# Kernel optimization log

Measured on AMD Instinct MI355X. Metric: run time of the kernel, lower is better.

The kernel has to match this reference:

```python
import jax, jax.numpy as jnp
import numpy as np

DIM = 64
LSH_NUM_PROJS = 7
BLOCK_SIZE = 256
SAMPLE_SIZE = 256
MIN_SEQ_LEN = 2048


def _unit_hamming(n):
    # Gray-code-like permutation used by AngularLSH so adjacent hash ids differ by 1 bit
    a = np.arange(2)
    for i in range(1, n):
        a = np.concatenate([a, a[::-1] + 2 ** i])
    return jnp.asarray(a, dtype=jnp.int32)

_PERM = _unit_hamming(LSH_NUM_PROJS)                                  # [2^P]
_ENC = (2 ** jnp.arange(LSH_NUM_PROJS)).reshape(1, 1, 1, LSH_NUM_PROJS)


def _lsh_hash(mat, proj_dir):
    # mat: [b,h,n,d], proj_dir: [1,1,d,P] -> hash ids [b,h,n]
    mask = jnp.matmul(mat, proj_dir) > 0
    bin_ids = (mask * _ENC).sum(-1)
    return _PERM[bin_ids]


def _exact_attention(q, k, v, scale, causal=False, bias=None):
    qk = jnp.einsum('bhnd,bhmd->bhnm', q, k) * scale
    if causal:
        n, m = q.shape[2], k.shape[2]
        qk = qk + jnp.triu(jnp.full((n, m), jnp.finfo(q.dtype).min, q.dtype), 1)[None, None]
    if bias is not None:
        qk = qk + bias
    lse = jax.scipy.special.logsumexp(qk, axis=-1, keepdims=True)      # [b,h,n,1]
    out = jnp.einsum('bhnm,bhmd->bhnd', jnp.exp(qk - lse), v)
    return out, lse


def _add_attn(a1, l1, a2, l2):
    c = (1.0 / (1.0 + jnp.exp(l2 - l1))).astype(a1.dtype)
    attn = c * a1 + (1 - c) * a2
    lse = l1 - jnp.log(c + jnp.finfo(l1.dtype).eps)
    return attn, lse


def _indexing(x, idx, chunk_size=-1):
    # x: [b,h,n,d], idx: [b,h,s] -> [b,h,s,d] (padded up to a multiple of chunk_size)
    g = jnp.take_along_axis(x, idx[..., None], axis=2)
    n = g.shape[2]
    if chunk_size > 0 and n % chunk_size != 0:
        pad = -n % chunk_size
        g = jnp.pad(g, ((0, 0), (0, 0), (0, pad), (0, 0)))
    return g


def _no_causal(q, k, v, scale, proj_dir, level):
    b, h, n_q, d = q.shape
    n_k = k.shape[2]
    if MIN_SEQ_LEN > n_q:
        return _exact_attention(q, k, v, scale, causal=False)
    q_idx = jnp.argsort(_lsh_hash(q, proj_dir), axis=2)
    k_idx = jnp.argsort(_lsh_hash(k, proj_dir), axis=2)
    q_idx_inv = jnp.argsort(q_idx, axis=2)
    kbs = BLOCK_SIZE
    q_s = _indexing(q, q_idx, kbs)
    k_s = _indexing(k, k_idx, kbs)
    v_s = _indexing(v, k_idx, kbs)
    num_blocks = k_s.shape[2] // kbs
    qbs = q_s.shape[2] // num_blocks
    # block-diagonal attention over LSH-sorted buckets
    q_blk = q_s.reshape(-1, 1, qbs, d)
    k_blk = k_s.reshape(-1, 1, kbs, d)
    v_blk = v_s.reshape(-1, 1, kbs, d)
    attn_block, lse_block = _exact_attention(q_blk, k_blk, v_blk, scale, causal=False)
    attn_block = attn_block.reshape(b, h, q_s.shape[2], -1)
    lse_block = lse_block.reshape(b, h, q_s.shape[2], -1)
    if q_s.shape[2] != n_q:
        attn_block = attn_block[:, :, :n_q, :]
        lse_block = lse_block[:, :, :n_q, :]
        q_s = q_s[:, :, :n_q, :]
        k_s = k_s[:, :, :n_k, :]
        v_s = v_s[:, :, :n_k, :]
    S = SAMPLE_SIZE
    if S > 0 and n_q > qbs and n_k > kbs:
        rng = jax.random.fold_in(jax.random.key(42), level)
        sampled = jax.random.randint(rng, (b, h, S), 0, n_k)
        v_sub = _indexing(v_s, sampled)
        k_sub = _indexing(k_s, sampled)
        offset = jnp.arange(n_q)[None, :, None]                         # (1,n,1)
        bm = (offset // qbs) == (sampled // kbs).reshape(-1, 1, S)      # (b*h,n,S)
        bias = bm.reshape(b, h, n_q, S).astype(q_s.dtype) * jnp.finfo(q_s.dtype).min
        attn_res, lse_res = _exact_attention(q_s, k_sub, v_sub, scale, causal=False, bias=bias)
        lse_res = lse_res + jnp.asarray(np.log(n_k / S), lse_res.dtype)
        attn, lse = _add_attn(attn_block, lse_block, attn_res, lse_res)
    else:
        attn, lse = attn_block, lse_block
    attn = _indexing(attn, q_idx_inv)
    lse = _indexing(lse, q_idx_inv)
    return attn, lse


def _hyper(q, k, v, scale, proj_dir, level=0):
    b, h, n_k, d = k.shape
    n_q = q.shape[2]
    if n_k <= MIN_SEQ_LEN:
        return _exact_attention(q, k, v, scale, causal=True)
    # recursive causal split: block-diagonal halves + un-masked lower-left quadrant
    q_bd = q.reshape(b, 2 * h, n_q // 2, d)
    k_bd = k.reshape(b, 2 * h, n_k // 2, d)
    v_bd = v.reshape(b, 2 * h, n_k // 2, d)
    attn_bd, lse_bd = _hyper(q_bd, k_bd, v_bd, scale, proj_dir, level + 1)
    attn_bd = attn_bd.reshape(b, h, -1, d)
    lse_bd = lse_bd.reshape(b, h, -1, 1)
    a_un, l_un = _no_causal(q[:, :, n_k // 2:, :], k[:, :, :n_k // 2, :],
                            v[:, :, :n_k // 2, :], scale, proj_dir, 100 + level)
    a_up, l_up = attn_bd[:, :, :n_q // 2, :], lse_bd[:, :, :n_q // 2, :]
    a_dn, l_dn = _add_attn(attn_bd[:, :, n_q // 2:, :], lse_bd[:, :, n_q // 2:, :], a_un, l_un)
    return jnp.concatenate([a_up, a_dn], axis=2), jnp.concatenate([l_up, l_dn], axis=2)


def setup_inputs() -> dict:
    rng = jax.random.key(0)
    kq, kk, kv, kp = jax.random.split(rng, 4)
    B, H, N, D = 1, 8, 8192, 64
    return {
        'query': jax.random.normal(kq, (B, H, N, D), jnp.float32),
        'key': jax.random.normal(kk, (B, H, N, D), jnp.float32),
        'value': jax.random.normal(kv, (B, H, N, D), jnp.float32),
        'proj_dir': jax.random.normal(kp, (1, 1, D, LSH_NUM_PROJS), jnp.float32),
    }


def reference(query, key, value, proj_dir):
    scale = query.shape[-1] ** -0.5
    attn, lse = _hyper(query, key, value, scale, proj_dir)
    return attn
```

## Files before the change

### kernel.cpp

```cpp
#include <hip/hip_runtime.h>
#include <stdint.h>
#include <math.h>

#define H 8
#define NSEQ 8192
#define D 64
#define SC2 0.18033688011112042f
#define LN2F 0.69314718055994531f
#define THR2 10.0f
#define EPSF 1.1920928955078125e-07f

typedef short v8s __attribute__((ext_vector_type(8)));
typedef float v4f __attribute__((ext_vector_type(4)));
typedef unsigned short ushort_t;

#define MFMA16(a,b,c) __builtin_amdgcn_mfma_f32_16x16x32_bf16((a),(b),(c),0,0,0)
#define SWZ(row, cb)    (((row)*128) + ((cb) ^ ((((row)&7))<<4)))
#define SWZ256(row, cb) (((row)*256) + ((cb) ^ ((((row)&7))<<4)))

__device__ __forceinline__ float exp2x(float x){
  float r; asm("v_exp_f32 %0, %1" : "=v"(r) : "v"(x)); return r;
}
__device__ __forceinline__ unsigned int cvtpk(float a, float b){
  unsigned int r; asm("v_cvt_pk_bf16_f32 %0, %1, %2" : "=v"(r) : "v"(a), "v"(b)); return r;
}
__device__ __forceinline__ ushort_t f2bf(float f){
  union { float f; unsigned int u; } c; c.f = f;
  unsigned int u = c.u + 0x7FFFu + ((c.u >> 16) & 1u);
  return (ushort_t)(u >> 16);
}
#define VONES (v8s){0x3F80,0x3F80,0x3F80,0x3F80,0x3F80,0x3F80,0x3F80,0x3F80}

__global__ __launch_bounds__(256) void prep_hash(
    const float* __restrict__ q, const float* __restrict__ k, const float* __restrict__ v,
    const float* __restrict__ proj,
    ushort_t* __restrict__ qb, ushort_t* __restrict__ kb, ushort_t* __restrict__ vb,
    int* __restrict__ hq, int* __restrict__ hk)
{
  __shared__ float tile[64][65];
  __shared__ float pj[448];
  __shared__ int pbuf[4][64];
  const int bid = blockIdx.x;
  const int t = threadIdx.x;
  if (bid >= 2048){
    const int tix = bid - 2048;
    size_t off = (size_t)tix*4096 + t*16;
    float4 f0 = *(const float4*)(v + off);
    float4 f1 = *(const float4*)(v + off + 4);
    float4 f2 = *(const float4*)(v + off + 8);
    float4 f3 = *(const float4*)(v + off + 12);
    uint4 o0, o1;
    o0.x = cvtpk(f0.x, f0.y);  o0.y = cvtpk(f0.z, f0.w);
    o0.z = cvtpk(f1.x, f1.y);  o0.w = cvtpk(f1.z, f1.w);
    o1.x = cvtpk(f2.x, f2.y);  o1.y = cvtpk(f2.z, f2.w);
    o1.z = cvtpk(f3.x, f3.y);  o1.w = cvtpk(f3.z, f3.w);
    *(uint4*)(vb + off) = o0;
    *(uint4*)(vb + off + 8) = o1;
    return;
  }
  const int isk = bid & 1;
  const int tix = bid >> 1;
  const int rowbase = tix << 6;
  const float* src = isk ? k : q;
  ushort_t* dstb = isk ? kb : qb;
  int* dsth = isk ? hk : hq;
  for (int i = t; i < 448; i += 256) pj[i] = proj[i];
  {
    const int r = t >> 2, cg = (t & 3) << 4;
    const float* s = src + (size_t)(rowbase + r)*64 + cg;
    float4 f0 = *(const float4*)(s);
    float4 f1 = *(const float4*)(s + 4);
    float4 f2 = *(const float4*)(s + 8);
    float4 f3 = *(const float4*)(s + 12);
    tile[r][cg+0]=f0.x;  tile[r][cg+1]=f0.y;  tile[r][cg+2]=f0.z;  tile[r][cg+3]=f0.w;
    tile[r][cg+4]=f1.x;  tile[r][cg+5]=f1.y;  tile[r][cg+6]=f1.z;  tile[r][cg+7]=f1.w;
    tile[r][cg+8]=f2.x;  tile[r][cg+9]=f2.y;  tile[r][cg+10]=f2.z; tile[r][cg+11]=f2.w;
    tile[r][cg+12]=f3.x; tile[r][cg+13]=f3.y; tile[r][cg+14]=f3.z; tile[r][cg+15]=f3.w;
    uint4 o0, o1;
    o0.x = cvtpk(f0.x, f0.y);  o0.y = cvtpk(f0.z, f0.w);
    o0.z = cvtpk(f1.x, f1.y);  o0.w = cvtpk(f1.z, f1.w);
    o1.x = cvtpk(f2.x, f2.y);  o1.y = cvtpk(f2.z, f2.w);
    o1.z = cvtpk(f3.x, f3.y);  o1.w = cvtpk(f3.z, f3.w);
    *(uint4*)(dstb + (size_t)(rowbase + r)*64 + cg) = o0;
    *(uint4*)(dstb + (size_t)(rowbase + r)*64 + cg + 8) = o1;
  }
  __syncthreads();
  {
    const int r = t & 63, pg = t >> 6;
    const int p2 = (pg < 3) ? (pg + 4) : 6;
    float d0 = 0.0f, d1 = 0.0f;
    for (int d = 0; d < 64; ++d){
      float x = tile[r][d];
      d0 = fmaf(x, pj[d*7 + pg], d0);
      d1 = fmaf(x, pj[d*7 + p2], d1);
    }
    int pb = (d0 > 0.0f ? (1 << pg) : 0);
    if (pg < 3 && d1 > 0.0f) pb |= (1 << (pg + 4));
    pbuf[pg][r] = pb;
  }
  __syncthreads();
  if (t < 64){
    int b = pbuf[0][t] | pbuf[1][t] | pbuf[2][t] | pbuf[3][t];
    dsth[rowbase + t] = b ^ (b >> 1);
  }
}

__device__ __forceinline__ void tf2x32(uint32_t k0, uint32_t k1,
                                       uint32_t x0, uint32_t x1,
                                       uint32_t& o0, uint32_t& o1)
{
  uint32_t ks0 = k0, ks1 = k1, ks2 = k0 ^ k1 ^ 0x1BD11BDAu;
  x0 += ks0; x1 += ks1;
#define RND(r) { x0 += x1; x1 = (x1 << (r)) | (x1 >> (32-(r))); x1 ^= x0; }
  RND(13) RND(15) RND(26) RND(6)  x0 += ks1; x1 += ks2 + 1u;
  RND(17) RND(29) RND(16) RND(24) x0 += ks2; x1 += ks0 + 2u;
  RND(13) RND(15) RND(26) RND(6)  x0 += ks0; x1 += ks1 + 3u;
  RND(17) RND(29) RND(16) RND(24) x0 += ks1; x1 += ks2 + 4u;
  RND(13) RND(15) RND(26) RND(6)  x0 += ks2; x1 += ks0 + 5u;
#undef RND
  o0 = x0; o1 = x1;
}

__device__ __forceinline__ void qk8(const v8s qf[2], const char* Ks, int lo, int hi, v4f sa[8]){
  __builtin_amdgcn_s_setprio(1);
#pragma unroll
  for (int st = 0; st < 8; ++st){
#pragma unroll
    for (int kc = 0; kc < 2; ++kc){
      v8s bf = *(const v8s*)(Ks + SWZ(st*16 + lo, kc*64 + hi*16));
      sa[st] = MFMA16(qf[kc], bf, sa[st]);
    }
  }
  __builtin_amdgcn_s_setprio(0);
}

__device__ __forceinline__ void sm_pv8s(v4f sa[8], char* Pw, const char* VTs,
                                        int lo, int hi, float m[4], v4f o[5]){
  float tm[4];
  bool grow = false;
#pragma unroll
  for (int reg = 0; reg < 4; ++reg){
    float a = fmaxf(fmaxf(sa[0][reg], sa[1][reg]), fmaxf(sa[2][reg], sa[3][reg]));
    float b = fmaxf(fmaxf(sa[4][reg], sa[5][reg]), fmaxf(sa[6][reg], sa[7][reg]));
    tm[reg] = fmaxf(a, b);
    grow = grow || (tm[reg] > m[reg] + THR2);
  }
  if (__any(grow)){
#pragma unroll
    for (int reg = 0; reg < 4; ++reg){
      float t = tm[reg];
      t = fmaxf(t, __shfl_xor(t, 1));
      t = fmaxf(t, __shfl_xor(t, 2));
      t = fmaxf(t, __shfl_xor(t, 4));
      t = fmaxf(t, __shfl_xor(t, 8));
      float mn = fmaxf(m[reg], t);
      float corr = exp2x(m[reg] - mn);
      m[reg] = mn;
#pragma unroll
      for (int dt = 0; dt < 5; ++dt) o[dt][reg] *= corr;
    }
  }
#pragma unroll
  for (int hh = 0; hh < 2; ++hh){
#pragma unroll
    for (int reg = 0; reg < 4; ++reg){
      float mr = m[reg];
      uint2 pw;
      pw.x = cvtpk(exp2x(sa[hh*4+0][reg]-mr), exp2x(sa[hh*4+1][reg]-mr));
      pw.y = cvtpk(exp2x(sa[hh*4+2][reg]-mr), exp2x(sa[hh*4+3][reg]-mr));
      *(uint2*)(Pw + SWZ(hi*4 + reg, 8*lo)) = pw;
    }
    asm volatile("" ::: "memory");
    __builtin_amdgcn_s_setprio(1);
#pragma unroll
    for (int kb = 0; kb < 2; ++kb){
      v8s pa = *(const v8s*)(Pw + SWZ(lo, kb*64 + hi*16));
#pragma unroll
      for (int dt = 0; dt < 4; ++dt){
        v8s vbr = *(const v8s*)(VTs + SWZ256(dt*16 + lo, hh*128 + kb*64 + hi*16));
        o[dt] = MFMA16(pa, vbr, o[dt]);
      }
      o[4] = MFMA16(pa, VONES, o[4]);
    }
    __builtin_amdgcn_s_setprio(0);
    asm volatile("" ::: "memory");
  }
}

__device__ __forceinline__ void vt_write_h(char* VTs, uint2 vr0, uint2 vr1, uint2 vr2, uint2 vr3,
                                           int vdg, int vlo, int vsth){
  const int cb = vsth*128 + vlo*8;
  uint2 w;
  w.x = (vr0.x & 0xFFFFu) | ((vr1.x & 0xFFFFu) << 16);
  w.y = (vr2.x & 0xFFFFu) | ((vr3.x & 0xFFFFu) << 16);
  *(uint2*)(VTs + SWZ256(vdg*4 + 0, cb)) = w;
  w.x = (vr0.x >> 16) | (vr1.x & 0xFFFF0000u);
  w.y = (vr2.x >> 16) | (vr3.x & 0xFFFF0000u);
  *(uint2*)(VTs + SWZ256(vdg*4 + 1, cb)) = w;
  w.x = (vr0.y & 0xFFFFu) | ((vr1.y & 0xFFFFu) << 16);
  w.y = (vr2.y & 0xFFFFu) | ((vr3.y & 0xFFFFu) << 16);
  *(uint2*)(VTs + SWZ256(vdg*4 + 2, cb)) = w;
  w.x = (vr0.y >> 16) | (vr1.y & 0xFFFF0000u);
  w.y = (vr2.y >> 16) | (vr3.y & 0xFFFF0000u);
  *(uint2*)(VTs + SWZ256(vdg*4 + 3, cb)) = w;
}

__global__ __launch_bounds__(512, 4) void diag_sort(
    const ushort_t* __restrict__ qb, const ushort_t* __restrict__ kb, const ushort_t* __restrict__ vb,
    float* __restrict__ out, float* __restrict__ lse,
    const int* __restrict__ hq, const int* __restrict__ hk,
    int* __restrict__ q100, int* __restrict__ k100,
    int* __restrict__ q101, int* __restrict__ k101,
    int* __restrict__ s100, int* __restrict__ s101)
{
  __shared__ __align__(16) char lds[49664];
  const int bid0 = blockIdx.x;
  const int tid = threadIdx.x;

  if (bid0 < 48){
    unsigned char  (*hist)[128] = (unsigned char (*)[128])lds;
    unsigned short (*off )[128] = (unsigned short(*)[128])(lds + 16384);
    int* bstart = (int*)(lds + 49152);
    const int t = tid;
    if (t < 128){
      int gid = bid0*128 + t;
      int level, span, idx; int* outp;
      if (gid < 2048){ level = 100; span = 4096; outp = s100; idx = gid; }
      else           { level = 101; span = 2048; outp = s101; idx = gid - 2048; }
      uint32_t r0, r1; tf2x32(0u, 42u, 0u, (uint32_t)level, r0, r1);
      uint32_t k20, k21; tf2x32(r0, r1, 0u, 1u, k20, k21);
      uint32_t o0, o1; tf2x32(k20, k21, 0u, (uint32_t)idx, o0, o1);
      outp[idx] = (int)((o0 ^ o1) % (uint32_t)span);
    }
    const int* src = nullptr; int n = 0, base = 0; int* outp = nullptr;
    if (bid0 < 8)       { int h = bid0;     src = hq + h*NSEQ + 4096;        n = 4096; base = 4096;          outp = q100 + h*4096; }
    else if (bid0 < 16) { int h = bid0 - 8; src = hk + h*NSEQ;               n = 4096; base = 0;             outp = k100 + h*4096; }
    else if (bid0 < 32) { int id = bid0-16; int h = id>>1, p = id&1;
                          src = hq + h*NSEQ + p*4096 + 2048;                 n = 2048; base = p*4096 + 2048; outp = q101 + id*2048; }
    else                { int id = bid0-32; int h = id>>1, p = id&1;
                          src = hk + h*NSEQ + p*4096;                        n = 2048; base = p*4096;       outp = k101 + id*2048; }
    const int chunk = n >> 7;
    if (t < 128) for (int b = 0; b < 128; ++b) hist[t][b] = 0;
    __syncthreads();
    const int* mysrc = src + (t & 127) * chunk;
    if (t < 128) for (int i = 0; i < chunk; ++i) hist[t][mysrc[i]]++;
    __syncthreads();
    if (t < 128){
      int s = 0;
      for (int tt = 0; tt < 128; ++tt) s += hist[tt][t];
      bstart[t] = s;
    }
    __syncthreads();
    if (t == 0){
      int run = 0;
      for (int b = 0; b < 128; ++b){ int c = bstart[b]; bstart[b] = run; run += c; }
    }
    __syncthreads();
    if (t < 128){
      unsigned int run = (unsigned int)bstart[t];
      for (int tt = 0; tt < 128; ++tt){ off[tt][t] = (unsigned short)run; run += hist[tt][t]; }
    }
    __syncthreads();
    if (t < 128){
      for (int i = 0; i < chunk; ++i){
        int hsh = mysrc[i];
        unsigned short pos = off[t][hsh]++;
        outp[pos] = base + t * chunk + i;
      }
    }
    return;
  }

  char* Ks  = lds;
  char* VTs = lds + 16384;
  char* Ps  = lds + 32768;
  const int bid = bid0 - 48;
  const int xcd = bid & 7, sl = bid >> 3;
  const int inst = xcd*4 + (sl >> 4);
  const int pi = sl & 15;
  const int h = inst >> 2, tblk = inst & 3;
  const size_t hoff = (size_t)h * NSEQ * D;
  const ushort_t* qh = qb + hoff; const ushort_t* kh = kb + hoff; const ushort_t* vh = vb + hoff;
  const int blkbase = tblk * 2048;
  const int w = tid >> 6, lane = tid & 63;
  const int lo = lane & 15, hi = lane >> 4;
  char* Pw = Ps + w*2048;
  const int kr = tid >> 2, kq = tid & 3;
  const int vlo = tid & 15, vdg = (tid >> 4) & 15, vsth = tid >> 8;

  const int qt  = (w < 4) ? (31 - pi) : pi;
  const int wq  = w & 3;
  const int nkt   = (31 - pi)/2 + 1;
  const int mynkt = qt/2 + 1;
  const int qpos0 = qt*64 + wq*16;

  v8s qf[2];
  {
    const ushort_t* r = qh + (size_t)(blkbase + qpos0 + lo) * D;
    qf[0] = *(const v8s*)(r + hi*8);
    qf[1] = *(const v8s*)(r + 32 + hi*8);
  }
  const v4f vz = {0.0f, 0.0f, 0.0f, 0.0f};
  v4f o[5] = {vz, vz, vz, vz, vz};
  float m[4] = {-INFINITY, -INFINITY, -INFINITY, -INFINITY};

  uint4 kreg0, kreg1; uint2 vr0, vr1, vr2, vr3;
#define DLOAD(kt) { \
    const ushort_t* ksr = kh + (size_t)(blkbase + (kt)*128 + kr)*D + kq*16; \
    kreg0 = *(const uint4*)ksr; \
    kreg1 = *(const uint4*)(ksr + 8); \
    const ushort_t* vs = vh + (size_t)(blkbase + (kt)*128 + vsth*64 + vlo)*D + vdg*4; \
    vr0 = *(const uint2*)(vs); \
    vr1 = *(const uint2*)(vs + 16*D); \
    vr2 = *(const uint2*)(vs + 32*D); \
    vr3 = *(const uint2*)(vs + 48*D); }

  DLOAD(0);
#pragma unroll 1
  for (int kt = 0; kt < nkt; ++kt){
    *(uint4*)(Ks + SWZ(kr, kq*32))      = kreg0;
    *(uint4*)(Ks + SWZ(kr, kq*32 + 16)) = kreg1;
    vt_write_h(VTs, vr0, vr1, vr2, vr3, vdg, vlo, vsth);
    __syncthreads();
    if (kt + 1 < nkt) DLOAD(kt+1);
    if (kt < mynkt){
      v4f sa[8] = {vz, vz, vz, vz, vz, vz, vz, vz};
      qk8(qf, Ks, lo, hi, sa);
#pragma unroll
      for (int st = 0; st < 8; ++st) sa[st] *= SC2;
      if (kt == mynkt - 1){
#pragma unroll
        for (int st = 0; st < 8; ++st){
          int kpos = kt*128 + st*16 + lo;
#pragma unroll
          for (int reg = 0; reg < 4; ++reg)
            if (kpos > qpos0 + hi*4 + reg) sa[st][reg] = -INFINITY;
        }
      }
      sm_pv8s(sa, Pw, VTs, lo, hi, m, o);
    }
    __syncthreads();
  }
#undef DLOAD
#pragma unroll
  for (int reg = 0; reg < 4; ++reg){
    int rw = blkbase + qpos0 + hi*4 + reg;
    float lsum = o[4][reg];
    float inv = 1.0f / lsum;
#pragma unroll
    for (int dt = 0; dt < 4; ++dt)
      out[hoff + (size_t)rw*D + dt*16 + lo] = o[dt][reg] * inv;
    if (lo == 0) lse[h*NSEQ + rw] = m[reg]*LN2F + logf(lsum);
  }
}

__global__ __launch_bounds__(512, 4) void nc_both(
    const ushort_t* __restrict__ qb, const ushort_t* __restrict__ kb, const ushort_t* __restrict__ vb,
    float* __restrict__ out, float* __restrict__ lse,
    const int* __restrict__ q101, const int* __restrict__ k101, const int* __restrict__ s101,
    const int* __restrict__ q100, const int* __restrict__ k100, const int* __restrict__ s100,
    ushort_t* __restrict__ a100, float* __restrict__ lse100)
{
  __shared__ __align__(16) char Ks[16384];
  __shared__ __align__(16) char VTs[16384];
  __shared__ __align__(16) char Ps[8][2048];
  __shared__ unsigned int ilds[512];
  const int bid = blockIdx.x;
  const bool lvl101 = bid < 256;
  int inst, jb; float delta2; int seglen;
  const int *qi, *ki, *sp;
  if (lvl101){
    int xcd = bid & 7, sl = bid >> 3; inst = xcd*2 + (sl >> 4); jb = sl & 15;
    delta2 = 3.0f; seglen = 2048;
    qi = q101 + inst*seglen; ki = k101 + inst*seglen; sp = s101 + inst*256;
  } else {
    int b2 = bid - 256; inst = b2 & 7; jb = b2 >> 3;
    delta2 = 4.0f; seglen = 4096;
    qi = q100 + inst*seglen; ki = k100 + inst*seglen; sp = s100 + inst*256;
  }
  const int h = lvl101 ? (inst >> 1) : inst;
  const int qblk = jb >> 1;
  const size_t hoff = (size_t)h * NSEQ * D;
  const ushort_t* qh = qb + hoff; const ushort_t* kh = kb + hoff; const ushort_t* vh = vb + hoff;
  const int tid = threadIdx.x;
  const int w = tid >> 6, lane = tid & 63;
  const int lo = lane & 15, hi = lane >> 4;
  char* Pw = Ps[w];
  const int kr = tid >> 2, kq = tid & 3;
  const int vlo = tid & 15, vdg = (tid >> 4) & 15, vsth = tid >> 8;

  {
    if (tid < 256){
      ilds[tid] = (unsigned int)ki[qblk*256 + tid];
    } else {
      int s = sp[tid - 256];
      unsigned int krow = (unsigned int)ki[s];
      if ((s >> 8) == qblk) krow |= 0x80000000u;
      ilds[tid] = krow;
    }
  }
  int orig[4];
  v8s qf[2];
  {
    int qrl = qi[jb*128 + w*16 + lo];
    const ushort_t* r = qh + (size_t)qrl * D;
    qf[0] = *(const v8s*)(r + hi*8);
    qf[1] = *(const v8s*)(r + 32 + hi*8);
#pragma unroll
    for (int reg = 0; reg < 4; ++reg) orig[reg] = qi[jb*128 + w*16 + hi*4 + reg];
  }
  const v4f vz = {0.0f, 0.0f, 0.0f, 0.0f};
  v4f o[5] = {vz, vz, vz, vz, vz};
  float m[4] = {-INFINITY, -INFINITY, -INFINITY, -INFINITY};
  __syncthreads();

  uint4 kreg0, kreg1; uint2 vr0, vr1, vr2, vr3;
#define NLOAD(kt) { \
    unsigned int krow = ilds[(kt)*128 + kr] & 0x7FFFFFFFu; \
    const ushort_t* ksr = kh + (size_t)krow*D + kq*16; \
    kreg0 = *(const uint4*)ksr; \
    kreg1 = *(const uint4*)(ksr + 8); \
    unsigned int g0 = ilds[(kt)*128 + vsth*64 + vlo     ] & 0x7FFFFFFFu; \
    unsigned int g1 = ilds[(kt)*128 + vsth*64 + 16 + vlo] & 0x7FFFFFFFu; \
    unsigned int g2 = ilds[(kt)*128 + vsth*64 + 32 + vlo] & 0x7FFFFFFFu; \
    unsigned int g3 = ilds[(kt)*128 + vsth*64 + 48 + vlo] & 0x7FFFFFFFu; \
    vr0 = *(const uint2*)(vh + (size_t)g0*D + vdg*4); \
    vr1 = *(const uint2*)(vh + (size_t)g1*D + vdg*4); \
    vr2 = *(const uint2*)(vh + (size_t)g2*D + vdg*4); \
    vr3 = *(const uint2*)(vh + (size_t)g3*D + vdg*4); }

  NLOAD(0);
#pragma unroll 1
  for (int kt = 0; kt < 4; ++kt){
    *(uint4*)(Ks + SWZ(kr, kq*32))      = kreg0;
    *(uint4*)(Ks + SWZ(kr, kq*32 + 16)) = kreg1;
    vt_write_h(VTs, vr0, vr1, vr2, vr3, vdg, vlo, vsth);
    __syncthreads();
    if (kt + 1 < 4) NLOAD(kt+1);
    v4f sa[8] = {vz, vz, vz, vz, vz, vz, vz, vz};
    qk8(qf, Ks, lo, hi, sa);
    if (kt < 2){
#pragma unroll
      for (int st = 0; st < 8; ++st) sa[st] *= SC2;
    } else {
#pragma unroll
      for (int st = 0; st < 8; ++st){
        if (ilds[kt*128 + st*16 + lo] >> 31) sa[st] = (v4f){-INFINITY, -INFINITY, -INFINITY, -INFINITY};
        else                                 sa[st] = sa[st]*SC2 + delta2;
      }
    }
    sm_pv8s(sa, Pw, VTs, lo, hi, m, o);
    __syncthreads();
  }
#undef NLOAD
  if (lvl101){
#pragma unroll
    for (int reg = 0; reg < 4; ++reg){
      int og = orig[reg];
      float lsum = o[4][reg];
      float l1v = lse[h*NSEQ + og];
      float l2v = m[reg]*LN2F + logf(lsum);
      float c = 1.0f / (1.0f + __expf(l2v - l1v));
      float inv = (1.0f - c) / lsum;
#pragma unroll
      for (int dt = 0; dt < 4; ++dt){
        float* ap = out + hoff + (size_t)og*D + dt*16 + lo;
        *ap = c * (*ap) + inv * o[dt][reg];
      }
      if (lo == 0) lse[h*NSEQ + og] = l1v - logf(c + EPSF);
    }
  } else {
#pragma unroll
    for (int reg = 0; reg < 4; ++reg){
      int og = orig[reg];
      float lsum = o[4][reg];
      float inv = 1.0f / lsum;
      ushort_t* arow = a100 + ((size_t)h*NSEQ + og)*D;
#pragma unroll
      for (int dt = 0; dt < 4; ++dt)
        arow[dt*16 + lo] = f2bf(o[dt][reg] * inv);
      if (lo == 0) lse100[h*NSEQ + og] = m[reg]*LN2F + logf(lsum);
    }
  }
}

__global__ __launch_bounds__(256) void merge_kernel(
    float* __restrict__ out, const float* __restrict__ lse,
    const ushort_t* __restrict__ a100, const float* __restrict__ lse100)
{
  const int gid = blockIdx.x * 256 + threadIdx.x;
  const size_t e = (size_t)gid * 4;
  const int h = (int)(e >> 18);
  const int rem = (int)(e & 262143);
  const int og = 4096 + (rem >> 6);
  const size_t row = (size_t)h*NSEQ + og;
  const float l1 = lse[row];
  const float l2 = lse100[row];
  const float c = 1.0f / (1.0f + __expf(l2 - l1));
  const float ic = 1.0f - c;
  float* op = out + ((size_t)h*NSEQ*D) + (size_t)og*D + (rem & 63);
  float4 ov = *(float4*)op;
  uint2 av = *(const uint2*)(a100 + row*D + (rem & 63));
  float a0 = __uint_as_float((av.x & 0xFFFFu) << 16);
  float a1 = __uint_as_float((av.x & 0xFFFF0000u));
  float a2 = __uint_as_float((av.y & 0xFFFFu) << 16);
  float a3 = __uint_as_float((av.y & 0xFFFF0000u));
  ov.x = c*ov.x + ic*a0;
  ov.y = c*ov.y + ic*a1;
  ov.z = c*ov.z + ic*a2;
  ov.w = c*ov.w + ic*a3;
  *(float4*)op = ov;
}

extern "C" void kernel_launch(void* const* d_in, const int* in_sizes, int n_in,
                              void* d_out, int out_size, void* d_ws, size_t ws_size,
                              hipStream_t stream)
{
  const float* q    = (const float*)d_in[0];
  const float* k    = (const float*)d_in[1];
  const float* v    = (const float*)d_in[2];
  const float* proj = (const float*)d_in[3];
  float* out = (float*)d_out;

  char* ws = (char*)d_ws;
  float* lse = (float*)ws;
  int* hq   = (int*)(ws + 262144);
  int* hk   = (int*)(ws + 524288);
  int* q100 = (int*)(ws + 786432);
  int* k100 = (int*)(ws + 917504);
  int* q101 = (int*)(ws + 1048576);
  int* k101 = (int*)(ws + 1179648);
  int* s100 = (int*)(ws + 1310720);
  int* s101 = (int*)(ws + 1318912);
  ushort_t* qb = (ushort_t*)(ws + 1335296);
  ushort_t* kb = qb + (size_t)H*NSEQ*D;
  ushort_t* vb = kb + (size_t)H*NSEQ*D;
  ushort_t* a100 = vb + (size_t)H*NSEQ*D;
  float* lse100 = (float*)(a100 + (size_t)H*NSEQ*D);

  prep_hash    <<<dim3(3072), dim3(256), 0, stream>>>(q, k, v, proj, qb, kb, vb, hq, hk);
  diag_sort    <<<dim3(560),  dim3(512), 0, stream>>>(qb, kb, vb, out, lse, hq, hk,
                                                      q100, k100, q101, k101, s100, s101);
  nc_both      <<<dim3(512),  dim3(512), 0, stream>>>(qb, kb, vb, out, lse,
                                                      q101, k101, s101, q100, k100, s100,
                                                      a100, lse100);
  merge_kernel <<<dim3(2048), dim3(256), 0, stream>>>(out, lse, a100, lse100);
}
```

Baseline: 99.10 us.

## Load V rows contiguously, transpose via scalar LDS stores, and rebalance block scheduling

V tiles are now fetched with the same contiguous 16-byte row loads as K, using the K row index. The transpose into the V^T LDS layout is done with 16 scalar 2-byte stores per thread instead of 4 packed 8-byte stores, which cuts the number of gathered global reads and index lookups, most notably in the sorted-index kernel. The diagonal kernel's block mapping is also reworked: sort blocks move to the end of the grid, and each block pairs query tiles 2j and 2j+1 so both wave groups share the same key-tile count, removing the per-wave mynkt skip. The tradeoff is more LDS store instructions and possible bank conflicts, plus a different XCD placement for the diagonal blocks.

```diff
diff --git a/kernel.cpp b/kernel.cpp
--- a/kernel.cpp
+++ b/kernel.cpp
@@ -187,22 +187,15 @@
   }
 }
 
-__device__ __forceinline__ void vt_write_h(char* VTs, uint2 vr0, uint2 vr1, uint2 vr2, uint2 vr3,
-                                           int vdg, int vlo, int vsth){
-  const int cb = vsth*128 + vlo*8;
-  uint2 w;
-  w.x = (vr0.x & 0xFFFFu) | ((vr1.x & 0xFFFFu) << 16);
-  w.y = (vr2.x & 0xFFFFu) | ((vr3.x & 0xFFFFu) << 16);
-  *(uint2*)(VTs + SWZ256(vdg*4 + 0, cb)) = w;
-  w.x = (vr0.x >> 16) | (vr1.x & 0xFFFF0000u);
-  w.y = (vr2.x >> 16) | (vr3.x & 0xFFFF0000u);
-  *(uint2*)(VTs + SWZ256(vdg*4 + 1, cb)) = w;
-  w.x = (vr0.y & 0xFFFFu) | ((vr1.y & 0xFFFFu) << 16);
-  w.y = (vr2.y & 0xFFFFu) | ((vr3.y & 0xFFFFu) << 16);
-  *(uint2*)(VTs + SWZ256(vdg*4 + 2, cb)) = w;
-  w.x = (vr0.y >> 16) | (vr1.y & 0xFFFF0000u);
-  w.y = (vr2.y >> 16) | (vr3.y & 0xFFFF0000u);
-  *(uint2*)(VTs + SWZ256(vdg*4 + 3, cb)) = w;
+__device__ __forceinline__ void vt_store_row(char* VTs, uint4 v0, uint4 v1, int kk, int qq){
+  const int vcolb = (kk >> 6)*128 + 2*(4*(kk & 15) + ((kk >> 4) & 3));
+  union { uint4 u; ushort_t s[8]; } a0, a1;
+  a0.u = v0; a1.u = v1;
+#pragma unroll
+  for (int dd = 0; dd < 8; ++dd){
+    *(ushort_t*)(VTs + SWZ256(qq*16 + dd, vcolb))     = a0.s[dd];
+    *(ushort_t*)(VTs + SWZ256(qq*16 + 8 + dd, vcolb)) = a1.s[dd];
+  }
 }
 
 __global__ __launch_bounds__(512, 4) void diag_sort(
@@ -217,13 +210,14 @@
   const int bid0 = blockIdx.x;
   const int tid = threadIdx.x;
 
-  if (bid0 < 48){
+  if (bid0 >= 512){
+    const int sbid = bid0 - 512;
     unsigned char  (*hist)[128] = (unsigned char (*)[128])lds;
     unsigned short (*off )[128] = (unsigned short(*)[128])(lds + 16384);
     int* bstart = (int*)(lds + 49152);
     const int t = tid;
     if (t < 128){
-      int gid = bid0*128 + t;
+      int gid = sbid*128 + t;
       int level, span, idx; int* outp;
       if (gid < 2048){ level = 100; span = 4096; outp = s100; idx = gid; }
       else           { level = 101; span = 2048; outp = s101; idx = gid - 2048; }
@@ -233,11 +227,11 @@
       outp[idx] = (int)((o0 ^ o1) % (uint32_t)span);
     }
     const int* src = nullptr; int n = 0, base = 0; int* outp = nullptr;
-    if (bid0 < 8)       { int h = bid0;     src = hq + h*NSEQ + 4096;        n = 4096; base = 4096;          outp = q100 + h*4096; }
-    else if (bid0 < 16) { int h = bid0 - 8; src = hk + h*NSEQ;               n = 4096; base = 0;             outp = k100 + h*4096; }
-    else if (bid0 < 32) { int id = bid0-16; int h = id>>1, p = id&1;
+    if (sbid < 8)       { int h = sbid;     src = hq + h*NSEQ + 4096;        n = 4096; base = 4096;          outp = q100 + h*4096; }
+    else if (sbid < 16) { int h = sbid - 8; src = hk + h*NSEQ;               n = 4096; base = 0;             outp = k100 + h*4096; }
+    else if (sbid < 32) { int id = sbid-16; int h = id>>1, p = id&1;
                           src = hq + h*NSEQ + p*4096 + 2048;                 n = 2048; base = p*4096 + 2048; outp = q101 + id*2048; }
-    else                { int id = bid0-32; int h = id>>1, p = id&1;
+    else                { int id = sbid-32; int h = id>>1, p = id&1;
                           src = hk + h*NSEQ + p*4096;                        n = 2048; base = p*4096;       outp = k101 + id*2048; }
     const int chunk = n >> 7;
     if (t < 128) for (int b = 0; b < 128; ++b) hist[t][b] = 0;
@@ -274,10 +268,10 @@
   char* Ks  = lds;
   char* VTs = lds + 16384;
   char* Ps  = lds + 32768;
-  const int bid = bid0 - 48;
-  const int xcd = bid & 7, sl = bid >> 3;
-  const int inst = xcd*4 + (sl >> 4);
-  const int pi = sl & 15;
+  int j;
+  if (bid0 < 256) j = 15 - (bid0 >> 5);
+  else            j = (bid0 - 256) >> 5;
+  const int inst = bid0 & 31;
   const int h = inst >> 2, tblk = inst & 3;
   const size_t hoff = (size_t)h * NSEQ * D;
   const ushort_t* qh = qb + hoff; const ushort_t* kh = kb + hoff; const ushort_t* vh = vb + hoff;
@@ -286,13 +280,10 @@
   const int lo = lane & 15, hi = lane >> 4;
   char* Pw = Ps + w*2048;
   const int kr = tid >> 2, kq = tid & 3;
-  const int vlo = tid & 15, vdg = (tid >> 4) & 15, vsth = tid >> 8;
-
-  const int qt  = (w < 4) ? (31 - pi) : pi;
-  const int wq  = w & 3;
-  const int nkt   = (31 - pi)/2 + 1;
-  const int mynkt = qt/2 + 1;
-  const int qpos0 = qt*64 + wq*16;
+
+  const int qt = (w < 4) ? (2*j + 1) : (2*j);
+  const int nkt = j + 1;
+  const int qpos0 = qt*64 + (w & 3)*16;
 
   v8s qf[2];
   {
@@ -304,31 +295,28 @@
   v4f o[5] = {vz, vz, vz, vz, vz};
   float m[4] = {-INFINITY, -INFINITY, -INFINITY, -INFINITY};
 
-  uint4 kreg0, kreg1; uint2 vr0, vr1, vr2, vr3;
+  uint4 kreg0, kreg1, vreg0, vreg1;
 #define DLOAD(kt) { \
-    const ushort_t* ksr = kh + (size_t)(blkbase + (kt)*128 + kr)*D + kq*16; \
-    kreg0 = *(const uint4*)ksr; \
-    kreg1 = *(const uint4*)(ksr + 8); \
-    const ushort_t* vs = vh + (size_t)(blkbase + (kt)*128 + vsth*64 + vlo)*D + vdg*4; \
-    vr0 = *(const uint2*)(vs); \
-    vr1 = *(const uint2*)(vs + 16*D); \
-    vr2 = *(const uint2*)(vs + 32*D); \
-    vr3 = *(const uint2*)(vs + 48*D); }
+    const size_t rb = (size_t)(blkbase + (kt)*128 + kr)*D + kq*16; \
+    kreg0 = *(const uint4*)(kh + rb); \
+    kreg1 = *(const uint4*)(kh + rb + 8); \
+    vreg0 = *(const uint4*)(vh + rb); \
+    vreg1 = *(const uint4*)(vh + rb + 8); }
 
   DLOAD(0);
 #pragma unroll 1
   for (int kt = 0; kt < nkt; ++kt){
     *(uint4*)(Ks + SWZ(kr, kq*32))      = kreg0;
     *(uint4*)(Ks + SWZ(kr, kq*32 + 16)) = kreg1;
-    vt_write_h(VTs, vr0, vr1, vr2, vr3, vdg, vlo, vsth);
+    vt_store_row(VTs, vreg0, vreg1, kr, kq);
     __syncthreads();
     if (kt + 1 < nkt) DLOAD(kt+1);
-    if (kt < mynkt){
+    {
       v4f sa[8] = {vz, vz, vz, vz, vz, vz, vz, vz};
       qk8(qf, Ks, lo, hi, sa);
 #pragma unroll
       for (int st = 0; st < 8; ++st) sa[st] *= SC2;
-      if (kt == mynkt - 1){
+      if (kt == nkt - 1){
 #pragma unroll
         for (int st = 0; st < 8; ++st){
           int kpos = kt*128 + st*16 + lo;
@@ -387,7 +375,6 @@
   const int lo = lane & 15, hi = lane >> 4;
   char* Pw = Ps[w];
   const int kr = tid >> 2, kq = tid & 3;
-  const int vlo = tid & 15, vdg = (tid >> 4) & 15, vsth = tid >> 8;
 
   {
     if (tid < 256){
@@ -414,27 +401,21 @@
   float m[4] = {-INFINITY, -INFINITY, -INFINITY, -INFINITY};
   __syncthreads();
 
-  uint4 kreg0, kreg1; uint2 vr0, vr1, vr2, vr3;
+  uint4 kreg0, kreg1, vreg0, vreg1;
 #define NLOAD(kt) { \
     unsigned int krow = ilds[(kt)*128 + kr] & 0x7FFFFFFFu; \
-    const ushort_t* ksr = kh + (size_t)krow*D + kq*16; \
-    kreg0 = *(const uint4*)ksr; \
-    kreg1 = *(const uint4*)(ksr + 8); \
-    unsigned int g0 = ilds[(kt)*128 + vsth*64 + vlo     ] & 0x7FFFFFFFu; \
-    unsigned int g1 = ilds[(kt)*128 + vsth*64 + 16 + vlo] & 0x7FFFFFFFu; \
-    unsigned int g2 = ilds[(kt)*128 + vsth*64 + 32 + vlo] & 0x7FFFFFFFu; \
-    unsigned int g3 = ilds[(kt)*128 + vsth*64 + 48 + vlo] & 0x7FFFFFFFu; \
-    vr0 = *(const uint2*)(vh + (size_t)g0*D + vdg*4); \
-    vr1 = *(const uint2*)(vh + (size_t)g1*D + vdg*4); \
-    vr2 = *(const uint2*)(vh + (size_t)g2*D + vdg*4); \
-    vr3 = *(const uint2*)(vh + (size_t)g3*D + vdg*4); }
+    const size_t rb = (size_t)krow*D + kq*16; \
+    kreg0 = *(const uint4*)(kh + rb); \
+    kreg1 = *(const uint4*)(kh + rb + 8); \
+    vreg0 = *(const uint4*)(vh + rb); \
+    vreg1 = *(const uint4*)(vh + rb + 8); }
 
   NLOAD(0);
 #pragma unroll 1
   for (int kt = 0; kt < 4; ++kt){
     *(uint4*)(Ks + SWZ(kr, kq*32))      = kreg0;
     *(uint4*)(Ks + SWZ(kr, kq*32 + 16)) = kreg1;
-    vt_write_h(VTs, vr0, vr1, vr2, vr3, vdg, vlo, vsth);
+    vt_store_row(VTs, vreg0, vreg1, kr, kq);
     __syncthreads();
     if (kt + 1 < 4) NLOAD(kt+1);
     v4f sa[8] = {vz, vz, vz, vz, vz, vz, vz, vz};
```

New measurement: 102.9 us. 1.04x slower.

## Pair adjacent query tiles per block and launch longest diagonal blocks first

Applied to the files above, without the earlier changes.

Each diagonal-attention block now handles the two query tiles 2j and 2j+1, which share the same number of 128-key tiles, in place of pairing tile pi with tile 31-pi. The per-wave early-exit and the separate mynkt bound go away. Blocks are ordered with the heaviest (largest j) first, and the LSH sort blocks move to the end of the grid. The intent is to remove idle waves inside a block and reduce imbalance through longest-first scheduling, at the cost of uneven per-block work across the grid. The XCD-aware mapping is dropped, which may change L2 locality.

```diff
diff --git a/kernel.cpp b/kernel.cpp
--- a/kernel.cpp
+++ b/kernel.cpp
@@ -217,13 +217,14 @@
   const int bid0 = blockIdx.x;
   const int tid = threadIdx.x;
 
-  if (bid0 < 48){
+  if (bid0 >= 512){
+    const int sbid = bid0 - 512;
     unsigned char  (*hist)[128] = (unsigned char (*)[128])lds;
     unsigned short (*off )[128] = (unsigned short(*)[128])(lds + 16384);
     int* bstart = (int*)(lds + 49152);
     const int t = tid;
     if (t < 128){
-      int gid = bid0*128 + t;
+      int gid = sbid*128 + t;
       int level, span, idx; int* outp;
       if (gid < 2048){ level = 100; span = 4096; outp = s100; idx = gid; }
       else           { level = 101; span = 2048; outp = s101; idx = gid - 2048; }
@@ -233,11 +234,11 @@
       outp[idx] = (int)((o0 ^ o1) % (uint32_t)span);
     }
     const int* src = nullptr; int n = 0, base = 0; int* outp = nullptr;
-    if (bid0 < 8)       { int h = bid0;     src = hq + h*NSEQ + 4096;        n = 4096; base = 4096;          outp = q100 + h*4096; }
-    else if (bid0 < 16) { int h = bid0 - 8; src = hk + h*NSEQ;               n = 4096; base = 0;             outp = k100 + h*4096; }
-    else if (bid0 < 32) { int id = bid0-16; int h = id>>1, p = id&1;
+    if (sbid < 8)       { int h = sbid;     src = hq + h*NSEQ + 4096;        n = 4096; base = 4096;          outp = q100 + h*4096; }
+    else if (sbid < 16) { int h = sbid - 8; src = hk + h*NSEQ;               n = 4096; base = 0;             outp = k100 + h*4096; }
+    else if (sbid < 32) { int id = sbid-16; int h = id>>1, p = id&1;
                           src = hq + h*NSEQ + p*4096 + 2048;                 n = 2048; base = p*4096 + 2048; outp = q101 + id*2048; }
-    else                { int id = bid0-32; int h = id>>1, p = id&1;
+    else                { int id = sbid-32; int h = id>>1, p = id&1;
                           src = hk + h*NSEQ + p*4096;                        n = 2048; base = p*4096;       outp = k101 + id*2048; }
     const int chunk = n >> 7;
     if (t < 128) for (int b = 0; b < 128; ++b) hist[t][b] = 0;
@@ -274,10 +275,10 @@
   char* Ks  = lds;
   char* VTs = lds + 16384;
   char* Ps  = lds + 32768;
-  const int bid = bid0 - 48;
-  const int xcd = bid & 7, sl = bid >> 3;
-  const int inst = xcd*4 + (sl >> 4);
-  const int pi = sl & 15;
+  int j;
+  if (bid0 < 256) j = 15 - (bid0 >> 5);
+  else            j = (bid0 - 256) >> 5;
+  const int inst = bid0 & 31;
   const int h = inst >> 2, tblk = inst & 3;
   const size_t hoff = (size_t)h * NSEQ * D;
   const ushort_t* qh = qb + hoff; const ushort_t* kh = kb + hoff; const ushort_t* vh = vb + hoff;
@@ -288,11 +289,9 @@
   const int kr = tid >> 2, kq = tid & 3;
   const int vlo = tid & 15, vdg = (tid >> 4) & 15, vsth = tid >> 8;
 
-  const int qt  = (w < 4) ? (31 - pi) : pi;
-  const int wq  = w & 3;
-  const int nkt   = (31 - pi)/2 + 1;
-  const int mynkt = qt/2 + 1;
-  const int qpos0 = qt*64 + wq*16;
+  const int qt = (w < 4) ? (2*j + 1) : (2*j);
+  const int nkt = j + 1;
+  const int qpos0 = qt*64 + (w & 3)*16;
 
   v8s qf[2];
   {
@@ -323,12 +322,12 @@
     vt_write_h(VTs, vr0, vr1, vr2, vr3, vdg, vlo, vsth);
     __syncthreads();
     if (kt + 1 < nkt) DLOAD(kt+1);
-    if (kt < mynkt){
+    {
       v4f sa[8] = {vz, vz, vz, vz, vz, vz, vz, vz};
       qk8(qf, Ks, lo, hi, sa);
 #pragma unroll
       for (int st = 0; st < 8; ++st) sa[st] *= SC2;
-      if (kt == mynkt - 1){
+      if (kt == nkt - 1){
 #pragma unroll
         for (int st = 0; st < 8; ++st){
           int kpos = kt*128 + st*16 + lo;
```

Result: no change. 100.0 us (+0.9%).
